# Kernel optimization log

Measured on AMD Instinct MI355X. Metric: run time of the kernel, lower is better.

## Reference

```python
import jax, jax.numpy as jnp
import numpy as np

B, S, D = 4, 2048, 2048
H, Dh, Dl = 16, 128, 128  # head_dim must equal latent_dim for the source matmul to type-check


def setup_inputs() -> dict:
    key = jax.random.key(0)
    ks = jax.random.split(key, 6)
    sc = 0.02
    return {
        "hidden_states": jax.random.normal(ks[0], (B, S, D), dtype=jnp.float32),
        "Wq": jax.random.normal(ks[1], (H * Dh, D), dtype=jnp.float32) * sc,
        "Wk_down": jax.random.normal(ks[2], (H * Dl, D), dtype=jnp.float32) * sc,
        "Wv_down": jax.random.normal(ks[3], (H * Dl, D), dtype=jnp.float32) * sc,
        "Wk_up": jax.random.normal(ks[4], (H * Dh, H * Dl), dtype=jnp.float32) * sc,
        "Wo": jax.random.normal(ks[5], (D, H * Dh), dtype=jnp.float32) * sc,
    }


def reference(hidden_states, Wq, Wk_down, Wv_down, Wk_up, Wo):
    # projections (torch Linear: y = x @ W.T)
    q = (hidden_states @ Wq.T).reshape(B, S, H, Dh).transpose(0, 2, 1, 3)        # [B,H,S,Dh]
    k_lat = (hidden_states @ Wk_down.T).reshape(B, S, H, Dl).transpose(0, 2, 1, 3)  # [B,H,S,Dl]
    v_lat = (hidden_states @ Wv_down.T).reshape(B, S, H, Dl).transpose(0, 2, 1, 3)  # [B,H,S,Dl]

    scores = jnp.einsum("bhsd,bhtd->bhst", q, k_lat) / jnp.sqrt(jnp.float32(Dl))
    attn = jax.nn.softmax(scores, axis=-1)
    out_lat = jnp.einsum("bhst,bhtd->bhsd", attn, v_lat)                          # [B,H,S,Dl]
    out_lat = out_lat.transpose(0, 2, 1, 3).reshape(B, S, H * Dl)

    # source bug (faithful): k_up_proj is applied to the attention output
    up = out_lat @ Wk_up.T                                                         # [B,S,H*Dh]
    return up @ Wo.T                                                               # [B,S,D]
```

## Files before the change

kernel.cpp:

```cpp
#include <hip/hip_runtime.h>
#include <hip/hip_bf16.h>
#include <stdint.h>

typedef unsigned short u16;
typedef __attribute__((ext_vector_type(4))) float f32x4;
typedef __attribute__((ext_vector_type(8))) short s16x8;
typedef __attribute__((ext_vector_type(4))) u16 u16x4;

__device__ __forceinline__ u16 f2bf(float x) {
  union { float f; uint32_t u; } v; v.f = x;
  uint32_t r = v.u + 0x7FFFu + ((v.u >> 16) & 1u);
  return (u16)(r >> 16);
}
__device__ __forceinline__ u16 f2bfh(float x) {
  __hip_bfloat16 h = __float2bfloat16(x);
  u16 r; __builtin_memcpy(&r, &h, 2); return r;
}

__device__ __forceinline__ void gload16(const void* g, const void* l) {
  __builtin_amdgcn_global_load_lds((const __attribute__((address_space(1))) void*)g,
                                   (__attribute__((address_space(3))) void*)l,
                                   16, 0, 0);
}

#define BAR() asm volatile("s_barrier" ::: "memory")
#define LGKM0() asm volatile("s_waitcnt lgkmcnt(0)" ::: "memory")
#define VMCNT4() asm volatile("s_waitcnt vmcnt(4)" ::: "memory")
#define VMCNT0() asm volatile("s_waitcnt vmcnt(0)" ::: "memory")

__global__ void fill_k(float* out, int n, float v) {
  for (int i = blockIdx.x * blockDim.x + threadIdx.x; i < n; i += gridDim.x * blockDim.x)
    out[i] = v;
}

__global__ void cvtall_k(const float* __restrict__ hs, const float* __restrict__ Wq,
                         const float* __restrict__ Wkd, const float* __restrict__ Wvd,
                         const float* __restrict__ Wo,
                         u16* __restrict__ hsB, u16* __restrict__ W3, u16* __restrict__ WoB) {
  int i = blockIdx.x * blockDim.x + threadIdx.x;
  const float* src; u16* dst; int off;
  if (i < 4194304)      { src = hs;  dst = hsB;          off = i; }
  else if (i < 5242880) { src = Wq;  dst = W3;           off = i - 4194304; }
  else if (i < 6291456) { src = Wkd; dst = W3 + 4194304; off = i - 5242880; }
  else if (i < 7340032) { src = Wvd; dst = W3 + 8388608; off = i - 6291456; }
  else                  { src = Wo;  dst = WoB;          off = i - 7340032; }
  f32x4 v = ((const f32x4*)src)[off];
  u16x4 o;
  o.x = f2bf(v.x); o.y = f2bf(v.y); o.z = f2bf(v.z); o.w = f2bf(v.w);
  ((u16x4*)dst)[off] = o;
}

__global__ void cvtT_k(const float* __restrict__ in, u16* __restrict__ out) {
  __shared__ float t[32][33];
  int tx = threadIdx.x, ty = threadIdx.y;
  int c = blockIdx.x * 32 + tx;
#pragma unroll
  for (int j = 0; j < 4; ++j) {
    int r = blockIdx.y * 32 + ty + j * 8;
    t[ty + j * 8][tx] = in[(size_t)r * 2048 + c];
  }
  __syncthreads();
  int c2 = blockIdx.y * 32 + tx;
#pragma unroll
  for (int j = 0; j < 4; ++j) {
    int r2 = blockIdx.x * 32 + ty + j * 8;
    out[(size_t)r2 * 2048 + c2] = f2bf(t[tx][ty + j * 8]);
  }
}

template <typename CT, int OUTMODE>
__global__ __launch_bounds__(256) void btgemm_k(const u16* __restrict__ A0,
                                                const u16* __restrict__ B0,
                                                CT* __restrict__ C,
                                                int M, int N, int K) {
  __shared__ u16 As[128 * 64];
  __shared__ u16 Bs[128 * 64];
  int nnt = N >> 7;
  int bid = blockIdx.x;
  int nwg = gridDim.x;
  if ((nwg & 7) == 0) { int q = nwg >> 3; bid = (bid & 7) * q + (bid >> 3); }
  int mt = bid / nnt, nt = bid - mt * nnt;
  int tid = threadIdx.x, wave = tid >> 6, lane = tid & 63;
  int l15 = lane & 15, l4 = lane >> 4;
  int wr = wave >> 1, wc = wave & 1;
  int sr = lane >> 3, sc = lane & 7;
  int gsl = (sc ^ sr) * 8;

  const u16* Ag = A0 + (size_t)(mt * 128 + wave * 32 + sr) * K + gsl;
  const u16* Bg = B0 + (size_t)(nt * 128 + wave * 32 + sr) * K + gsl;
  u16* Asw = As + wave * 32 * 64;
  u16* Bsw = Bs + wave * 32 * 64;

  f32x4 acc[4][4];
#pragma unroll
  for (int i = 0; i < 4; ++i)
#pragma unroll
    for (int j = 0; j < 4; ++j) acc[i][j] = f32x4{0.f, 0.f, 0.f, 0.f};

  for (int kt = 0; kt < K; kt += 64) {
#pragma unroll
    for (int i = 0; i < 4; ++i) {
      gload16(Ag + kt + i * 8 * K, Asw + i * 512);
      gload16(Bg + kt + i * 8 * K, Bsw + i * 512);
    }
    __syncthreads();
#pragma unroll
    for (int kk = 0; kk < 2; ++kk) {
      s16x8 af[4], bfr[4];
#pragma unroll
      for (int mf = 0; mf < 4; ++mf) {
        int row = wr * 64 + mf * 16 + l15;
        int sl = ((kk * 4 + l4) ^ (row & 7)) * 8;
        af[mf] = *(const s16x8*)(As + row * 64 + sl);
      }
#pragma unroll
      for (int nf = 0; nf < 4; ++nf) {
        int row = wc * 64 + nf * 16 + l15;
        int sl = ((kk * 4 + l4) ^ (row & 7)) * 8;
        bfr[nf] = *(const s16x8*)(Bs + row * 64 + sl);
      }
#pragma unroll
      for (int mf = 0; mf < 4; ++mf)
#pragma unroll
        for (int nf = 0; nf < 4; ++nf)
          acc[mf][nf] = __builtin_amdgcn_mfma_f32_16x16x32_bf16(af[mf], bfr[nf], acc[mf][nf], 0, 0, 0);
    }
    __syncthreads();
  }

  int crow = mt * 128 + wr * 64 + l4 * 4;
  int ccol = nt * 128 + wc * 64 + l15;
#pragma unroll
  for (int mf = 0; mf < 4; ++mf)
#pragma unroll
    for (int nf = 0; nf < 4; ++nf)
#pragma unroll
      for (int r = 0; r < 4; ++r) {
        size_t idx = (size_t)(crow + mf * 16 + r) * N + (ccol + nf * 16);
        float v = acc[mf][nf][r];
        if constexpr (OUTMODE == 0) C[idx] = v; else C[idx] = f2bfh(v);
      }
}

template <int MTILES, int NTILES, int OUTM>
__global__ __launch_bounds__(512, 2) void gemm256_k(const u16* __restrict__ A0,
                                                    const u16* __restrict__ B0,
                                                    u16* __restrict__ qk,
                                                    u16* __restrict__ Vt,
                                                    float* __restrict__ C) {
  __shared__ u16 lds4[4][2][8192];

  const int K = 2048;
  int bid = blockIdx.x;
  int bid2 = (bid & 7) * (MTILES * NTILES / 8) + (bid >> 3);
  int mt = bid2 / NTILES, nt = bid2 - mt * NTILES;
  int tid = threadIdx.x, wave = tid >> 6, lane = tid & 63;
  int l15 = lane & 15, l4 = lane >> 4;
  int wr = wave >> 2, wc = wave & 3;

  int rowin = tid >> 2;
  int gsl = (tid & 3) ^ (rowin & 3) ^ ((rowin >> 2) & 3);
  const u16* Agst = A0 + (size_t)(mt * 256 + rowin) * K + gsl * 8;
  const u16* Bgst = B0 + (size_t)(nt * 256 + rowin) * K + gsl * 8;
  const size_t HSTRIDE = (size_t)128 * K;

  int sl = l4 ^ (l15 & 3) ^ ((l15 >> 2) & 3);
  int aoff = wr * 4096 + l15 * 32 + sl * 8;
  int boff = wc * 2048 + l15 * 32 + sl * 8;

  f32x4 acc[8][4];
#pragma unroll
  for (int i = 0; i < 8; ++i)
#pragma unroll
    for (int j = 0; j < 4; ++j) acc[i][j] = f32x4{0.f, 0.f, 0.f, 0.f};

#pragma unroll
  for (int p = 0; p < 3; ++p) {
    gload16(Agst + p * 32, &lds4[p][0][wave * 512]);
    gload16(Agst + HSTRIDE + p * 32, &lds4[p][0][4096 + wave * 512]);
    gload16(Bgst + p * 32, &lds4[p][1][wave * 512]);
    gload16(Bgst + HSTRIDE + p * 32, &lds4[p][1][4096 + wave * 512]);
  }
  VMCNT4();
  BAR();

  s16x8 afc[4], afn[4], bfr0[4], bfr1[4];
#pragma unroll
  for (int i = 0; i < 4; ++i) {
    afc[i] = *(const s16x8*)(&lds4[0][0][0] + aoff + i * 512);
    bfr0[i] = *(const s16x8*)(&lds4[0][1][0] + boff + i * 512);
  }

#define TILE_STEP(T, BFC, BFN)                                                           \
  {                                                                                      \
    const u16* Ab = lds4[(T) & 3][0];                                                    \
    const u16* Abn = lds4[((T) + 1) & 3][0];                                             \
    const u16* Bbn = lds4[((T) + 1) & 3][1];                                             \
    int tt = ((T) + 3) & 63;                                                             \
    int sb = tt & 3;                                                                     \
    _Pragma("unroll") for (int i3 = 0; i3 < 4; ++i3)                                     \
      afn[i3] = *(const s16x8*)(Ab + aoff + (i3 + 4) * 512);                             \
    gload16(Agst + tt * 32, &lds4[sb][0][wave * 512]);                                   \
    gload16(Agst + HSTRIDE + tt * 32, &lds4[sb][0][4096 + wave * 512]);                  \
    gload16(Bgst + tt * 32, &lds4[sb][1][wave * 512]);                                   \
    gload16(Bgst + HSTRIDE + tt * 32, &lds4[sb][1][4096 + wave * 512]);                  \
    __builtin_amdgcn_s_setprio(1);                                                       \
    _Pragma("unroll") for (int mf = 0; mf < 4; ++mf)                                     \
      _Pragma("unroll") for (int nf = 0; nf < 4; ++nf)                                   \
        acc[mf][nf] = __builtin_amdgcn_mfma_f32_16x16x32_bf16(afc[mf], BFC[nf],          \
                                                              acc[mf][nf], 0, 0, 0);    \
    __builtin_amdgcn_s_setprio(0);                                                       \
    _Pragma("unroll") for (int i3 = 0; i3 < 4; ++i3) {                                   \
      afc[i3] = *(const s16x8*)(Abn + aoff + i3 * 512);                                  \
      BFN[i3] = *(const s16x8*)(Bbn + boff + i3 * 512);                                  \
    }                                                                                    \
    __builtin_amdgcn_s_setprio(1);                                                       \
    _Pragma("unroll") for (int mf = 0; mf < 4; ++mf)                                     \
      _Pragma("unroll") for (int nf = 0; nf < 4; ++nf)                                   \
        acc[mf + 4][nf] = __builtin_amdgcn_mfma_f32_16x16x32_bf16(afn[mf], BFC[nf],      \
                                                                  acc[mf + 4][nf], 0, 0, 0); \
    __builtin_amdgcn_s_setprio(0);                                                       \
    VMCNT4();                                                                            \
    BAR();                                                                               \
  }

  for (int t2 = 0; t2 < 32; ++t2) {
    TILE_STEP(2 * t2, bfr0, bfr1)
    TILE_STEP(2 * t2 + 1, bfr1, bfr0)
  }
#undef TILE_STEP
  VMCNT0();

  int crow0 = mt * 256 + wr * 128 + l4 * 4;
  int ccol0 = nt * 256 + wc * 64 + l15;
#pragma unroll
  for (int mf = 0; mf < 8; ++mf)
#pragma unroll
    for (int nf = 0; nf < 4; ++nf) {
      int col = ccol0 + nf * 16;
      int row0 = crow0 + mf * 16;
      if constexpr (OUTM == 1) {
#pragma unroll
        for (int r = 0; r < 4; ++r)
          C[(size_t)(row0 + r) * (NTILES * 256) + col] = acc[mf][nf][r];
      } else {
        if (col >= 4096) {
          int h = (col - 4096) >> 7, dh = (col - 4096) & 127;
          int b = row0 >> 11, s0 = row0 & 2047;
          u16x4 w;
          w.x = f2bfh(acc[mf][nf][0]); w.y = f2bfh(acc[mf][nf][1]);
          w.z = f2bfh(acc[mf][nf][2]); w.w = f2bfh(acc[mf][nf][3]);
          *(u16x4*)(Vt + ((size_t)((b << 4) + h) * 128 + dh) * 2048 + s0) = w;
        } else {
#pragma unroll
          for (int r = 0; r < 4; ++r)
            qk[(size_t)(row0 + r) * 4096 + col] = f2bfh(acc[mf][nf][r]);
        }
      }
    }
}

__global__ __launch_bounds__(512, 4) void attn11_k(const u16* __restrict__ qk,
                                                   const u16* __restrict__ Vt,
                                                   u16* __restrict__ outl) {
  __shared__ u16 Ks[2][64 * 128];
  __shared__ u16 Vs[2][128 * 64];
  __shared__ u16 Ps2[8 * 16 * 64];

  int bid = blockIdx.x;
  int xcd = bid & 7, slot = bid >> 3;
  int bh = xcd * 8 + (slot >> 4), qb = slot & 15;
  int b = bh >> 4, h = bh & 15;
  int tid = threadIdx.x, wave = tid >> 6, lane = tid & 63;
  int l15 = lane & 15, l4 = lane >> 4;
  int q0 = qb * 128 + wave * 16;
  const float ksc = 0.12751743f;

  s16x8 qf[4];
#pragma unroll
  for (int kf = 0; kf < 4; ++kf)
    qf[kf] = *(const s16x8*)(qk + (size_t)(b * 2048 + q0 + l15) * 4096 +
                             h * 128 + kf * 32 + l4 * 8);

  f32x4 po[8];
  float lrun = 0.f;
#pragma unroll
  for (int n2 = 0; n2 < 8; ++n2) po[n2] = f32x4{0.f, 0.f, 0.f, 0.f};

  char* PsW = (char*)Ps2 + wave * 2048;

  int krow_b = wave * 8;
  int vrow_b = wave * 16;
  int kj = lane & 15;
  int vj = lane & 7;

  s16x8 kr[2], vr[2];
#define GLOAD_TILE(kv0)                                                                  \
  _Pragma("unroll") for (int i = 0; i < 2; ++i) {                                        \
    int row = krow_b + i * 4 + (lane >> 4);                                              \
    kr[i] = *(const s16x8*)(qk + (size_t)(b * 2048 + (kv0) + row) * 4096 + 2048 +        \
                            h * 128 + kj * 8);                                           \
    int row2 = vrow_b + i * 8 + (lane >> 3);                                             \
    vr[i] = *(const s16x8*)(Vt + (size_t)(bh * 128 + row2) * 2048 + (kv0) + vj * 8);     \
  }

  GLOAD_TILE(0)

  for (int t = 0; t < 32; ++t) {
    int cur = t & 1;
    u16* Ksc = Ks[cur];
    u16* Vsc = Vs[cur];
#pragma unroll
    for (int i = 0; i < 2; ++i) {
      int row = krow_b + i * 4 + (lane >> 4);
      *(s16x8*)(Ksc + row * 128 + ((kj ^ (row & 7)) * 8)) = kr[i];
      int row2 = vrow_b + i * 8 + (lane >> 3);
      *(s16x8*)(Vsc + row2 * 64 + ((vj ^ (row2 & 7)) * 8)) = vr[i];
    }
    if (t < 31) GLOAD_TILE((t + 1) * 64)
    LGKM0();
    BAR();

    f32x4 sa[4];
#pragma unroll
    for (int nf = 0; nf < 4; ++nf) sa[nf] = f32x4{0.f, 0.f, 0.f, 0.f};
    __builtin_amdgcn_s_setprio(1);
#pragma unroll
    for (int kf = 0; kf < 4; ++kf) {
      s16x8 kb[4];
#pragma unroll
      for (int nf = 0; nf < 4; ++nf) {
        int row = nf * 16 + l15;
        int sl = ((kf * 4 + l4) ^ (row & 7)) * 8;
        kb[nf] = *(const s16x8*)(Ksc + row * 128 + sl);
      }
#pragma unroll
      for (int nf = 0; nf < 4; ++nf)
        sa[nf] = __builtin_amdgcn_mfma_f32_16x16x32_bf16(kb[nf], qf[kf], sa[nf], 0, 0, 0);
    }
    __builtin_amdgcn_s_setprio(0);

    {
      int row = l15;
      int swz = (row & 7) << 4;
#pragma unroll
      for (int nf = 0; nf < 4; ++nf) {
        float p0 = exp2f(sa[nf][0] * ksc);
        float p1 = exp2f(sa[nf][1] * ksc);
        float p2 = exp2f(sa[nf][2] * ksc);
        float p3 = exp2f(sa[nf][3] * ksc);
        lrun += (p0 + p1) + (p2 + p3);
        u16x4 w;
        w.x = f2bfh(p0); w.y = f2bfh(p1); w.z = f2bfh(p2); w.w = f2bfh(p3);
        *(u16x4*)(PsW + row * 128 + (((nf * 4 + l4) * 8) ^ swz)) = w;
      }
    }

    s16x8 pb[2];
    {
      int row = l15;
      int swz = (row & 7) << 4;
#pragma unroll
      for (int k2 = 0; k2 < 2; ++k2)
        pb[k2] = *(const s16x8*)(PsW + row * 128 + ((k2 * 64 + l4 * 16) ^ swz));
    }

    __builtin_amdgcn_s_setprio(1);
#pragma unroll
    for (int n2 = 0; n2 < 8; ++n2) {
#pragma unroll
      for (int k2 = 0; k2 < 2; ++k2) {
        int row = n2 * 16 + l15;
        int sl = ((k2 * 4 + l4) ^ (row & 7)) * 8;
        s16x8 vb = *(const s16x8*)(Vsc + row * 64 + sl);
        po[n2] = __builtin_amdgcn_mfma_f32_16x16x32_bf16(vb, pb[k2], po[n2], 0, 0, 0);
      }
    }
    __builtin_amdgcn_s_setprio(0);
  }
#undef GLOAD_TILE

  {
    lrun += __shfl_xor(lrun, 16, 64);
    lrun += __shfl_xor(lrun, 32, 64);
    float inv = 1.0f / lrun;
#pragma unroll
    for (int n2 = 0; n2 < 8; ++n2) {
      u16x4 w;
      w.x = f2bfh(po[n2][0] * inv);
      w.y = f2bfh(po[n2][1] * inv);
      w.z = f2bfh(po[n2][2] * inv);
      w.w = f2bfh(po[n2][3] * inv);
      *(u16x4*)(outl + (size_t)(b * 2048 + q0 + l15) * 2048 + h * 128 + n2 * 16 + l4 * 4) = w;
    }
  }
}

extern "C" void kernel_launch(void* const* d_in, const int* in_sizes, int n_in,
                              void* d_out, int out_size, void* d_ws, size_t ws_size,
                              hipStream_t stream) {
  (void)in_sizes; (void)n_in;
  const float* hs  = (const float*)d_in[0];
  const float* Wq  = (const float*)d_in[1];
  const float* Wkd = (const float*)d_in[2];
  const float* Wvd = (const float*)d_in[3];
  const float* Wku = (const float*)d_in[4];
  const float* Wo  = (const float*)d_in[5];
  float* out = (float*)d_out;
  char* ws = (char*)d_ws;

  if (ws_size < 201326592ull) {
    fill_k<<<4096, 256, 0, stream>>>(out, out_size, 1e9f);
    return;
  }

  u16* W3   = (u16*)(ws);
  u16* WcH  = (u16*)(ws + 25165824);
  u16* hsB  = (u16*)(ws + 33554432);
  u16* outl = (u16*)(ws + 33554432);
  u16* qk   = (u16*)(ws + 67108864);
  u16* WoB  = (u16*)(ws + 134217728);
  u16* WkuT = (u16*)(ws + 142606336);
  u16* Vt   = (u16*)(ws + 167772160);

  cvtall_k<<<32768, 256, 0, stream>>>(hs, Wq, Wkd, Wvd, Wo, hsB, W3, WoB);
  cvtT_k<<<dim3(64, 64), dim3(32, 8), 0, stream>>>(Wku, WkuT);

  btgemm_k<u16, 1><<<256, 256, 0, stream>>>(WoB, WkuT, WcH, 2048, 2048, 2048);

  gemm256_k<32, 24, 0><<<768, 512, 0, stream>>>(hsB, W3, qk, Vt, nullptr);

  attn11_k<<<1024, 512, 0, stream>>>(qk, Vt, outl);

  gemm256_k<32, 8, 1><<<256, 512, 0, stream>>>(outl, WcH, nullptr, nullptr, out);
}
```

Before: 501.5 us.

## Load GEMM B operand straight from global into registers, bypassing LDS

In the 256x256 bf16 GEMM, the B-operand tile is no longer staged through LDS. Each wave now reads its B fragments straight from global memory into registers, one K-tile ahead, and the vmcnt wait is raised to match the extra in-flight loads. This halves the kernel's LDS footprint, which may allow two blocks per CU, and removes B's LDS write and read traffic. The trade-offs are a much shorter prefetch distance for B, duplicate B loads across the two wave rows, and a past-the-end read on the final iteration.

```diff
diff --git a/kernel.cpp b/kernel.cpp
--- a/kernel.cpp
+++ b/kernel.cpp
@@ -25,7 +25,7 @@
 
 #define BAR() asm volatile("s_barrier" ::: "memory")
 #define LGKM0() asm volatile("s_waitcnt lgkmcnt(0)" ::: "memory")
-#define VMCNT4() asm volatile("s_waitcnt vmcnt(4)" ::: "memory")
+#define VMCNT6() asm volatile("s_waitcnt vmcnt(6)" ::: "memory")
 #define VMCNT0() asm volatile("s_waitcnt vmcnt(0)" ::: "memory")
 
 __global__ void fill_k(float* out, int n, float v) {
@@ -148,7 +148,7 @@
                                                     u16* __restrict__ qk,
                                                     u16* __restrict__ Vt,
                                                     float* __restrict__ C) {
-  __shared__ u16 lds4[4][2][8192];
+  __shared__ u16 lds4[4][8192];
 
   const int K = 2048;
   int bid = blockIdx.x;
@@ -161,12 +161,12 @@
   int rowin = tid >> 2;
   int gsl = (tid & 3) ^ (rowin & 3) ^ ((rowin >> 2) & 3);
   const u16* Agst = A0 + (size_t)(mt * 256 + rowin) * K + gsl * 8;
-  const u16* Bgst = B0 + (size_t)(nt * 256 + rowin) * K + gsl * 8;
   const size_t HSTRIDE = (size_t)128 * K;
+
+  const u16* Bfrag = B0 + (size_t)(nt * 256 + wc * 64 + l15) * K + l4 * 8;
 
   int sl = l4 ^ (l15 & 3) ^ ((l15 >> 2) & 3);
   int aoff = wr * 4096 + l15 * 32 + sl * 8;
-  int boff = wc * 2048 + l15 * 32 + sl * 8;
 
   f32x4 acc[8][4];
 #pragma unroll
@@ -176,51 +176,47 @@
 
 #pragma unroll
   for (int p = 0; p < 3; ++p) {
-    gload16(Agst + p * 32, &lds4[p][0][wave * 512]);
-    gload16(Agst + HSTRIDE + p * 32, &lds4[p][0][4096 + wave * 512]);
-    gload16(Bgst + p * 32, &lds4[p][1][wave * 512]);
-    gload16(Bgst + HSTRIDE + p * 32, &lds4[p][1][4096 + wave * 512]);
-  }
-  VMCNT4();
+    gload16(Agst + p * 32, &lds4[p][wave * 512]);
+    gload16(Agst + HSTRIDE + p * 32, &lds4[p][4096 + wave * 512]);
+  }
+  s16x8 afc[4], afn[4], bfr0[4], bfr1[4];
+#pragma unroll
+  for (int nf = 0; nf < 4; ++nf)
+    bfr0[nf] = *(const s16x8*)(Bfrag + (size_t)nf * 16 * K);
+  VMCNT6();
   BAR();
 
-  s16x8 afc[4], afn[4], bfr0[4], bfr1[4];
-#pragma unroll
-  for (int i = 0; i < 4; ++i) {
-    afc[i] = *(const s16x8*)(&lds4[0][0][0] + aoff + i * 512);
-    bfr0[i] = *(const s16x8*)(&lds4[0][1][0] + boff + i * 512);
-  }
+#pragma unroll
+  for (int i = 0; i < 4; ++i)
+    afc[i] = *(const s16x8*)(&lds4[0][0] + aoff + i * 512);
 
 #define TILE_STEP(T, BFC, BFN)                                                           \
   {                                                                                      \
-    const u16* Ab = lds4[(T) & 3][0];                                                    \
-    const u16* Abn = lds4[((T) + 1) & 3][0];                                             \
-    const u16* Bbn = lds4[((T) + 1) & 3][1];                                             \
+    const u16* Ab = lds4[(T) & 3];                                                       \
+    const u16* Abn = lds4[((T) + 1) & 3];                                                \
     int tt = ((T) + 3) & 63;                                                             \
     int sb = tt & 3;                                                                     \
     _Pragma("unroll") for (int i3 = 0; i3 < 4; ++i3)                                     \
       afn[i3] = *(const s16x8*)(Ab + aoff + (i3 + 4) * 512);                             \
-    gload16(Agst + tt * 32, &lds4[sb][0][wave * 512]);                                   \
-    gload16(Agst + HSTRIDE + tt * 32, &lds4[sb][0][4096 + wave * 512]);                  \
-    gload16(Bgst + tt * 32, &lds4[sb][1][wave * 512]);                                   \
-    gload16(Bgst + HSTRIDE + tt * 32, &lds4[sb][1][4096 + wave * 512]);                  \
+    gload16(Agst + tt * 32, &lds4[sb][wave * 512]);                                      \
+    gload16(Agst + HSTRIDE + tt * 32, &lds4[sb][4096 + wave * 512]);                     \
     __builtin_amdgcn_s_setprio(1);                                                       \
     _Pragma("unroll") for (int mf = 0; mf < 4; ++mf)                                     \
       _Pragma("unroll") for (int nf = 0; nf < 4; ++nf)                                   \
         acc[mf][nf] = __builtin_amdgcn_mfma_f32_16x16x32_bf16(afc[mf], BFC[nf],          \
                                                               acc[mf][nf], 0, 0, 0);    \
     __builtin_amdgcn_s_setprio(0);                                                       \
-    _Pragma("unroll") for (int i3 = 0; i3 < 4; ++i3) {                                   \
+    _Pragma("unroll") for (int i3 = 0; i3 < 4; ++i3)                                     \
       afc[i3] = *(const s16x8*)(Abn + aoff + i3 * 512);                                  \
-      BFN[i3] = *(const s16x8*)(Bbn + boff + i3 * 512);                                  \
-    }                                                                                    \
+    _Pragma("unroll") for (int nf = 0; nf < 4; ++nf)                                     \
+      BFN[nf] = *(const s16x8*)(Bfrag + (size_t)nf * 16 * K + ((T) + 1) * 32);           \
     __builtin_amdgcn_s_setprio(1);                                                       \
     _Pragma("unroll") for (int mf = 0; mf < 4; ++mf)                                     \
       _Pragma("unroll") for (int nf = 0; nf < 4; ++nf)                                   \
         acc[mf + 4][nf] = __builtin_amdgcn_mfma_f32_16x16x32_bf16(afn[mf], BFC[nf],      \
                                                                   acc[mf + 4][nf], 0, 0, 0); \
     __builtin_amdgcn_s_setprio(0);                                                       \
-    VMCNT4();                                                                            \
+    VMCNT6();                                                                            \
     BAR();                                                                               \
   }
 
```

New measurement: 604.8 us. 1.21x slower.
